# Optimization experiments

Hardware: AMD Instinct MI355X
Metric: run time of the kernel (lower is better)

## Reference

```python
import jax, jax.numpy as jnp
import numpy as np

N_NODES = 50000
N_HYPEREDGES = 50000
E = 320000
D = 256


def _prelu(x, a):
    return jnp.where(x >= 0, x, a * x)


def _hypergraph_conv(x, hei, W, b, num_nodes, num_edges):
    # PyG HypergraphConv, use_attention=False, heads=1:
    # out = D^{-1} H B^{-1} H^T (X W^T) + b
    src = hei[0]  # node indices, [E]
    he = hei[1]   # hyperedge indices, [E]
    xw = x @ W.T  # [N, D] node transform (lin has no bias)
    ones = jnp.ones((hei.shape[1],), x.dtype)
    deg_n = jax.ops.segment_sum(ones, src, num_segments=num_nodes)   # node degree D
    deg_e = jax.ops.segment_sum(ones, he, num_segments=num_edges)    # hyperedge size B
    d_inv = jnp.where(deg_n > 0, 1.0 / deg_n, 0.0)
    b_inv = jnp.where(deg_e > 0, 1.0 / deg_e, 0.0)
    # node -> hyperedge aggregation, scaled by B^{-1}
    edge_feat = b_inv[:, None] * jax.ops.segment_sum(xw[src], he, num_segments=num_edges)  # [n_he, D]
    # hyperedge -> node aggregation, scaled by D^{-1}
    out = d_inv[:, None] * jax.ops.segment_sum(edge_feat[he], src, num_segments=num_nodes)  # [N, D]
    return out + b


def setup_inputs() -> dict:
    key = jax.random.key(0)
    ks = jax.random.split(key, 6)
    std = np.sqrt(2.0 / D)  # kaiming_normal
    x = jax.random.normal(ks[0], (N_NODES, D), dtype=jnp.float32)
    hyper_edge_index = jax.random.randint(ks[1], (2, E), 0, N_HYPEREDGES, dtype=jnp.int64)
    W1 = jax.random.normal(ks[2], (D, D), dtype=jnp.float32) * std
    b1 = jnp.zeros((D,), jnp.float32)
    W2 = jax.random.normal(ks[3], (D, D), dtype=jnp.float32) * std
    b2 = jnp.zeros((D,), jnp.float32)
    prelu_a = jnp.asarray(0.25, jnp.float32)
    return {"x": x, "W1": W1, "b1": b1, "W2": W2, "b2": b2,
            "prelu_a": prelu_a, "hyper_edge_index": hyper_edge_index}


def reference(x, W1, b1, W2, b2, prelu_a, hyper_edge_index):
    out = _hypergraph_conv(x, hyper_edge_index, W1, b1, N_NODES, N_HYPEREDGES)
    out = _prelu(out, prelu_a)
    out = _hypergraph_conv(out, hyper_edge_index, W2, b2, N_NODES, N_HYPEREDGES)
    out = out + x  # residual
    out = _prelu(out, prelu_a)
    return out
```

## Files before the change

kernel.cpp:

```cpp
#include <hip/hip_runtime.h>

#define NN    50000
#define NHE   50000
#define NEDGE 320000
#define DD    256

#define SB    1024
#define NBLK  ((NN + SB - 1) / SB)
#define CNTB  ((NEDGE / 4 + 255) / 256)
#define XCB   (NN * DD / 2048)

typedef float f32x4 __attribute__((ext_vector_type(4)));
typedef short short8 __attribute__((ext_vector_type(8)));

static __device__ __forceinline__ unsigned short f2b(float f) {
    union { float f; unsigned u; } c; c.f = f;
    unsigned u = c.u;
    u += 0x7fffu + ((u >> 16) & 1u);
    return (unsigned short)(u >> 16);
}
static __device__ __forceinline__ float b2f_lo(unsigned v) {
    union { unsigned u; float f; } c; c.u = v << 16; return c.f;
}
static __device__ __forceinline__ float b2f_hi(unsigned v) {
    union { unsigned u; float f; } c; c.u = v & 0xffff0000u; return c.f;
}
static __device__ __forceinline__ unsigned pack2(float a, float b) {
    return (unsigned)f2b(a) | ((unsigned)f2b(b) << 16);
}

static __device__ __forceinline__ void glds16(const unsigned short* g, unsigned short* l) {
    __builtin_amdgcn_global_load_lds((const __attribute__((address_space(1))) unsigned int*)g,
                                     (__attribute__((address_space(3))) unsigned int*)l,
                                     16, 0, 0);
}

__global__ __launch_bounds__(256) void k_count_cvt(const int* __restrict__ src,
                                                   const int* __restrict__ he,
                                                   int* __restrict__ cnt_n,
                                                   int* __restrict__ cnt_e,
                                                   int* __restrict__ rank_n,
                                                   int* __restrict__ rank_e,
                                                   const float* __restrict__ w1,
                                                   const float* __restrict__ w2,
                                                   unsigned short* __restrict__ o1,
                                                   unsigned short* __restrict__ o2,
                                                   const float* __restrict__ x,
                                                   unsigned short* __restrict__ xb) {
    int bx = blockIdx.x;
    if (bx >= CNTB + 128) {
        int t = (bx - CNTB - 128) * 256 + threadIdx.x;
        const float4* p = (const float4*)x + (size_t)t * 2;
        float4 a = p[0], b = p[1];
        uint4 o;
        o.x = pack2(a.x, a.y); o.y = pack2(a.z, a.w);
        o.z = pack2(b.x, b.y); o.w = pack2(b.z, b.w);
        ((uint4*)xb)[t] = o;
        return;
    }
    if (bx >= CNTB) {
        int t = (bx - CNTB) * 256 + threadIdx.x;
        const int n4 = DD * DD / 4;
        const float* s = (t < n4) ? w1 : w2;
        unsigned short* d = (t < n4) ? o1 : o2;
        int i = (t < n4) ? t : t - n4;
        float4 v = ((const float4*)s)[i];
        uint2 o;
        o.x = pack2(v.x, v.y);
        o.y = pack2(v.z, v.w);
        ((uint2*)d)[i] = o;
        return;
    }
    int t  = bx * 256 + threadIdx.x;
    int e0 = t * 4;
    if (e0 >= NEDGE) return;
    int4 s = *(const int4*)(src + e0);
    int4 h = *(const int4*)(he + e0);
    int4 rn, re;
    rn.x = atomicAdd(&cnt_n[s.x], 1);
    rn.y = atomicAdd(&cnt_n[s.y], 1);
    rn.z = atomicAdd(&cnt_n[s.z], 1);
    rn.w = atomicAdd(&cnt_n[s.w], 1);
    re.x = atomicAdd(&cnt_e[h.x], 1);
    re.y = atomicAdd(&cnt_e[h.y], 1);
    re.z = atomicAdd(&cnt_e[h.z], 1);
    re.w = atomicAdd(&cnt_e[h.w], 1);
    *(int4*)(rank_n + e0) = rn;
    *(int4*)(rank_e + e0) = re;
}

__global__ __launch_bounds__(256) void k_scan(const int* __restrict__ cnt_n,
                                              const int* __restrict__ cnt_e,
                                              int* __restrict__ off_n,
                                              int* __restrict__ off_e) {
    int b   = blockIdx.x;
    int seg = b / NBLK, lb = b % NBLK;
    const int* cnt = seg ? cnt_e : cnt_n;
    int* off = seg ? off_e : off_n;
    int t = threadIdx.x;

    int pre = lb * SB;
    int s = 0;
    for (int i = t * 4; i < pre; i += 1024) {
        int4 c = *(const int4*)(cnt + i);
        s += c.x + c.y + c.z + c.w;
    }
    __shared__ int red[256];
    red[t] = s;
    __syncthreads();
    for (int o = 128; o > 0; o >>= 1) {
        if (t < o) red[t] += red[t + o];
        __syncthreads();
    }
    int base = red[0];

    int idx = pre + t * 4;
    int v[4];
    int tsum = 0;
#pragma unroll
    for (int j = 0; j < 4; ++j) {
        v[j] = (idx + j < NN) ? cnt[idx + j] : 0;
        tsum += v[j];
    }
    __shared__ int sc[256];
    sc[t] = tsum;
    __syncthreads();
    for (int o = 1; o < 256; o <<= 1) {
        int val = (t >= o) ? sc[t - o] : 0;
        __syncthreads();
        sc[t] += val;
        __syncthreads();
    }
    int p = base + sc[t] - tsum;
#pragma unroll
    for (int j = 0; j < 4; ++j) {
        if (idx + j < NN) off[idx + j] = p;
        p += v[j];
    }
    if (lb == NBLK - 1 && t == 255) off[NN] = base + sc[255];
}

__global__ __launch_bounds__(256) void k_fill(const int* __restrict__ src,
                                              const int* __restrict__ he,
                                              const int* __restrict__ off_n,
                                              const int* __restrict__ off_e,
                                              const int* __restrict__ rank_n,
                                              const int* __restrict__ rank_e,
                                              int* __restrict__ adj_n,
                                              int* __restrict__ adj_e) {
    int t  = blockIdx.x * 256 + threadIdx.x;
    int e0 = t * 4;
    if (e0 >= NEDGE) return;
    int4 s  = *(const int4*)(src + e0);
    int4 h  = *(const int4*)(he + e0);
    int4 rn = *(const int4*)(rank_n + e0);
    int4 re = *(const int4*)(rank_e + e0);
    int on0 = off_n[s.x], on1 = off_n[s.y], on2 = off_n[s.z], on3 = off_n[s.w];
    int oe0 = off_e[h.x], oe1 = off_e[h.y], oe2 = off_e[h.z], oe3 = off_e[h.w];
    adj_n[on0 + rn.x] = h.x;
    adj_n[on1 + rn.y] = h.y;
    adj_n[on2 + rn.z] = h.z;
    adj_n[on3 + rn.w] = h.w;
    adj_e[oe0 + re.x] = s.x;
    adj_e[oe1 + re.y] = s.y;
    adj_e[oe2 + re.z] = s.z;
    adj_e[oe3 + re.w] = s.w;
}

__global__ __launch_bounds__(1024) void k_gemm(const unsigned short* __restrict__ Av,
                                               const unsigned short* __restrict__ Wb,
                                               unsigned short* __restrict__ Cb) {
    __shared__ __align__(16) unsigned short Bs[128 * 256];
    const int t    = threadIdx.x;
    const int lane = t & 63;
    const int wave = t >> 6;
    const int n0   = (blockIdx.x & 1) * 128;
    const int fr   = lane & 15;
    const int fq   = lane >> 4;

#pragma unroll
    for (int q = 0; q < 4; ++q) {
        int row   = q * 32 + wave * 2 + (lane >> 5);
        int chunk = lane & 31;
        glds16(Wb + (size_t)(n0 + row) * DD + ((chunk ^ (row & 7)) * 8),
               Bs + q * 8192 + wave * 512);
    }

    int mchunk = (blockIdx.x >> 1) * 16 + wave;
    int m0  = mchunk * 16;
    int m0c = (m0 + 16 <= NN) ? m0 : NN - 16;
    short8 af[8];
    {
        const unsigned short* p = Av + (size_t)(m0c + fr) * DD + fq * 8;
#pragma unroll
        for (int kc = 0; kc < 8; ++kc)
            af[kc] = *(const short8*)(p + kc * 32);
    }

    __syncthreads();
    if (m0 >= NN) return;

    f32x4 acc[8] = {};
#pragma unroll
    for (int kc = 0; kc < 8; ++kc) {
#pragma unroll
        for (int nt = 0; nt < 8; ++nt) {
            int r  = nt * 16 + fr;
            int ch = (kc * 4 + fq) ^ (fr & 7);
            short8 bf = *(const short8*)(Bs + r * 256 + ch * 8);
            acc[nt] = __builtin_amdgcn_mfma_f32_16x16x32_bf16(af[kc], bf, acc[nt], 0, 0, 0);
        }
    }

#pragma unroll
    for (int nt = 0; nt < 8; ++nt)
#pragma unroll
        for (int i = 0; i < 4; ++i)
            Cb[(size_t)(m0 + fq * 4 + i) * DD + n0 + nt * 16 + fr] = f2b(acc[nt][i]);
}

static __device__ __forceinline__ void acc8(float* a, uint4 v) {
    a[0] += b2f_lo(v.x); a[1] += b2f_hi(v.x);
    a[2] += b2f_lo(v.y); a[3] += b2f_hi(v.y);
    a[4] += b2f_lo(v.z); a[5] += b2f_hi(v.z);
    a[6] += b2f_lo(v.w); a[7] += b2f_hi(v.w);
}
static __device__ __forceinline__ void gather8(const unsigned short* __restrict__ srcb,
                                               const int* __restrict__ adj,
                                               int b, int e, int sl, float* a) {
#pragma unroll
    for (int i = 0; i < 8; ++i) a[i] = 0.f;
    for (int i = b; i < e; i += 8) {
        int g0 = adj[i];
        int g[8];
        g[0] = g0;
#pragma unroll
        for (int j = 1; j < 8; ++j) g[j] = (i + j < e) ? adj[i + j] : g0;
        uint4 v[8];
#pragma unroll
        for (int j = 0; j < 8; ++j)
            v[j] = *(const uint4*)(srcb + (size_t)g[j] * DD + sl * 8);
        acc8(a, v[0]);
#pragma unroll
        for (int j = 1; j < 8; ++j)
            if (i + j < e) acc8(a, v[j]);
    }
}

__global__ __launch_bounds__(256) void k_gather_edge_b(const unsigned short* __restrict__ xw,
                                                       unsigned short* __restrict__ ef,
                                                       const int* __restrict__ off,
                                                       const int* __restrict__ adj) {
    int tid = blockIdx.x * 256 + threadIdx.x;
    int w = tid >> 5;
    int sl = tid & 31;
    if (w >= NHE) return;
    int b = off[w], e = off[w + 1];
    float a[8];
    gather8(xw, adj, b, e, sl, a);
    float sc = (e > b) ? 1.f / (float)(e - b) : 0.f;
    uint4 o;
    o.x = pack2(a[0] * sc, a[1] * sc);
    o.y = pack2(a[2] * sc, a[3] * sc);
    o.z = pack2(a[4] * sc, a[5] * sc);
    o.w = pack2(a[6] * sc, a[7] * sc);
    *(uint4*)(ef + (size_t)w * DD + sl * 8) = o;
}

__global__ __launch_bounds__(256) void k_gather_node_mid_b(const unsigned short* __restrict__ ef,
                                                           unsigned short* __restrict__ h,
                                                           const int* __restrict__ off,
                                                           const int* __restrict__ adj,
                                                           const float* __restrict__ bias,
                                                           const float* __restrict__ aP) {
    int tid = blockIdx.x * 256 + threadIdx.x;
    int w = tid >> 5;
    int sl = tid & 31;
    if (w >= NN) return;
    int b = off[w], e = off[w + 1];
    float a[8];
    gather8(ef, adj, b, e, sl, a);
    float sc = (e > b) ? 1.f / (float)(e - b) : 0.f;
    float al = *aP;
    float4 bb0 = ((const float4*)bias)[sl * 2];
    float4 bb1 = ((const float4*)bias)[sl * 2 + 1];
    float r[8];
    r[0] = a[0] * sc + bb0.x; r[1] = a[1] * sc + bb0.y;
    r[2] = a[2] * sc + bb0.z; r[3] = a[3] * sc + bb0.w;
    r[4] = a[4] * sc + bb1.x; r[5] = a[5] * sc + bb1.y;
    r[6] = a[6] * sc + bb1.z; r[7] = a[7] * sc + bb1.w;
#pragma unroll
    for (int i = 0; i < 8; ++i) r[i] = (r[i] >= 0.f) ? r[i] : al * r[i];
    uint4 o;
    o.x = pack2(r[0], r[1]);
    o.y = pack2(r[2], r[3]);
    o.z = pack2(r[4], r[5]);
    o.w = pack2(r[6], r[7]);
    *(uint4*)(h + (size_t)w * DD + sl * 8) = o;
}

__global__ __launch_bounds__(256) void k_gather_node_final_b(const unsigned short* __restrict__ ef,
                                                             const float* __restrict__ x,
                                                             float* __restrict__ out,
                                                             const int* __restrict__ off,
                                                             const int* __restrict__ adj,
                                                             const float* __restrict__ bias,
                                                             const float* __restrict__ aP) {
    int tid = blockIdx.x * 256 + threadIdx.x;
    int w = tid >> 5;
    int sl = tid & 31;
    if (w >= NN) return;
    int b = off[w], e = off[w + 1];
    float a[8];
    gather8(ef, adj, b, e, sl, a);
    float sc = (e > b) ? 1.f / (float)(e - b) : 0.f;
    float al = *aP;
    float4 bb0 = ((const float4*)bias)[sl * 2];
    float4 bb1 = ((const float4*)bias)[sl * 2 + 1];
    const float* xp = x + (size_t)w * DD + sl * 8;
    float4 xv0 = *(const float4*)xp;
    float4 xv1 = *(const float4*)(xp + 4);
    float r[8];
    r[0] = a[0] * sc + bb0.x + xv0.x; r[1] = a[1] * sc + bb0.y + xv0.y;
    r[2] = a[2] * sc + bb0.z + xv0.z; r[3] = a[3] * sc + bb0.w + xv0.w;
    r[4] = a[4] * sc + bb1.x + xv1.x; r[5] = a[5] * sc + bb1.y + xv1.y;
    r[6] = a[6] * sc + bb1.z + xv1.z; r[7] = a[7] * sc + bb1.w + xv1.w;
#pragma unroll
    for (int i = 0; i < 8; ++i) r[i] = (r[i] >= 0.f) ? r[i] : al * r[i];
    float* op = out + (size_t)w * DD + sl * 8;
    *(float4*)op = make_float4(r[0], r[1], r[2], r[3]);
    *(float4*)(op + 4) = make_float4(r[4], r[5], r[6], r[7]);
}

extern "C" void kernel_launch(void* const* d_in, const int* in_sizes, int n_in,
                              void* d_out, int out_size, void* d_ws, size_t ws_size,
                              hipStream_t stream) {
    const float* x       = (const float*)d_in[0];
    const float* W1      = (const float*)d_in[1];
    const float* b1      = (const float*)d_in[2];
    const float* W2      = (const float*)d_in[3];
    const float* b2      = (const float*)d_in[4];
    const float* prelu_a = (const float*)d_in[5];
    const int*   hei     = (const int*)d_in[6];
    const int* idx_src = hei;
    const int* idx_he  = hei + NEDGE;

    float* out = (float*)d_out;
    unsigned short* B1 = (unsigned short*)d_ws;
    unsigned short* B2 = B1 + (size_t)NN * DD;
    int* off_n  = (int*)(B2 + (size_t)NN * DD);
    int* off_e  = off_n + NN + 1;
    int* cnt_n  = off_e + NHE + 1;
    int* cnt_e  = cnt_n + NN;
    int* adj_n  = cnt_e + NHE;
    int* adj_e  = adj_n + NEDGE;
    int* rank_n = adj_e + NEDGE;
    int* rank_e = rank_n + NEDGE;
    unsigned short* w1b = (unsigned short*)d_out;
    unsigned short* w2b = w1b + DD * DD;

    const int gblocks = (NN * 32 + 255) / 256;
    const int gemmb   = 2 * (NN / 16 / 16 + 1);

    hipMemsetAsync(cnt_n, 0, sizeof(int) * (NN + NHE), stream);
    k_count_cvt<<<CNTB + 128 + XCB, 256, 0, stream>>>(idx_src, idx_he, cnt_n, cnt_e,
                                                      rank_n, rank_e, W1, W2, w1b, w2b,
                                                      x, B2);
    k_scan<<<2 * NBLK, 256, 0, stream>>>(cnt_n, cnt_e, off_n, off_e);
    k_fill<<<CNTB, 256, 0, stream>>>(idx_src, idx_he, off_n, off_e,
                                     rank_n, rank_e, adj_n, adj_e);

    k_gemm<<<gemmb, 1024, 0, stream>>>(B2, w1b, B1);
    k_gather_edge_b<<<gblocks, 256, 0, stream>>>(B1, B2, off_e, adj_e);
    k_gather_node_mid_b<<<gblocks, 256, 0, stream>>>(B2, B1, off_n, adj_n, b1, prelu_a);

    k_gemm<<<gemmb, 1024, 0, stream>>>(B1, w2b, B2);
    k_gather_edge_b<<<gblocks, 256, 0, stream>>>(B2, B1, off_e, adj_e);
    k_gather_node_final_b<<<gblocks, 256, 0, stream>>>(B1, x, out, off_n, adj_n, b2, prelu_a);
}
```

Measured before the change: 306.4 us.

## Split degree counters into four sub-buckets to reduce atomic contention

The per-node and per-hyperedge degree counters are replaced by four interleaved sub-counters per index, chosen from the block id, so concurrent atomics from different blocks land on different addresses. The scan now also emits a base offset for each sub-bucket, and the fill kernel uses those bases plus the recorded rank to place adjacency entries. The counters live in the B1 workspace before the GEMM overwrites it. This trades atomic contention for a fourfold larger counter array, a larger memset, and more scan traffic.

Result: slower. 323.8 us (+5.7%).

```diff
diff --git a/kernel.cpp b/kernel.cpp
--- a/kernel.cpp
+++ b/kernel.cpp
@@ -9,6 +9,7 @@
 #define NBLK  ((NN + SB - 1) / SB)
 #define CNTB  ((NEDGE / 4 + 255) / 256)
 #define XCB   (NN * DD / 2048)
+#define NBKT  100000
 
 typedef float f32x4 __attribute__((ext_vector_type(4)));
 typedef short short8 __attribute__((ext_vector_type(8)));
@@ -37,8 +38,7 @@
 
 __global__ __launch_bounds__(256) void k_count_cvt(const int* __restrict__ src,
                                                    const int* __restrict__ he,
-                                                   int* __restrict__ cnt_n,
-                                                   int* __restrict__ cnt_e,
+                                                   int* __restrict__ cntI,
                                                    int* __restrict__ rank_n,
                                                    int* __restrict__ rank_e,
                                                    const float* __restrict__ w1,
@@ -74,35 +74,37 @@
     int t  = bx * 256 + threadIdx.x;
     int e0 = t * 4;
     if (e0 >= NEDGE) return;
+    int r = bx & 3;
     int4 s = *(const int4*)(src + e0);
     int4 h = *(const int4*)(he + e0);
     int4 rn, re;
-    rn.x = atomicAdd(&cnt_n[s.x], 1);
-    rn.y = atomicAdd(&cnt_n[s.y], 1);
-    rn.z = atomicAdd(&cnt_n[s.z], 1);
-    rn.w = atomicAdd(&cnt_n[s.w], 1);
-    re.x = atomicAdd(&cnt_e[h.x], 1);
-    re.y = atomicAdd(&cnt_e[h.y], 1);
-    re.z = atomicAdd(&cnt_e[h.z], 1);
-    re.w = atomicAdd(&cnt_e[h.w], 1);
+    rn.x = atomicAdd(&cntI[s.x * 4 + r], 1);
+    rn.y = atomicAdd(&cntI[s.y * 4 + r], 1);
+    rn.z = atomicAdd(&cntI[s.z * 4 + r], 1);
+    rn.w = atomicAdd(&cntI[s.w * 4 + r], 1);
+    re.x = atomicAdd(&cntI[(50000 + h.x) * 4 + r], 1);
+    re.y = atomicAdd(&cntI[(50000 + h.y) * 4 + r], 1);
+    re.z = atomicAdd(&cntI[(50000 + h.z) * 4 + r], 1);
+    re.w = atomicAdd(&cntI[(50000 + h.w) * 4 + r], 1);
     *(int4*)(rank_n + e0) = rn;
     *(int4*)(rank_e + e0) = re;
 }
 
-__global__ __launch_bounds__(256) void k_scan(const int* __restrict__ cnt_n,
-                                              const int* __restrict__ cnt_e,
+__global__ __launch_bounds__(256) void k_scan(const int* __restrict__ cntI,
                                               int* __restrict__ off_n,
-                                              int* __restrict__ off_e) {
+                                              int* __restrict__ off_e,
+                                              int* __restrict__ baseI) {
     int b   = blockIdx.x;
     int seg = b / NBLK, lb = b % NBLK;
-    const int* cnt = seg ? cnt_e : cnt_n;
+    const int4* cnt4 = (const int4*)cntI + (size_t)seg * 50000;
+    int4* base4 = (int4*)baseI + (size_t)seg * 50000;
     int* off = seg ? off_e : off_n;
     int t = threadIdx.x;
 
     int pre = lb * SB;
     int s = 0;
-    for (int i = t * 4; i < pre; i += 1024) {
-        int4 c = *(const int4*)(cnt + i);
+    for (int i = t; i < pre; i += 256) {
+        int4 c = cnt4[i];
         s += c.x + c.y + c.z + c.w;
     }
     __shared__ int red[256];
@@ -115,12 +117,14 @@
     int base = red[0];
 
     int idx = pre + t * 4;
-    int v[4];
+    int4 cv[4];
+    int tot[4];
     int tsum = 0;
 #pragma unroll
     for (int j = 0; j < 4; ++j) {
-        v[j] = (idx + j < NN) ? cnt[idx + j] : 0;
-        tsum += v[j];
+        cv[j] = (idx + j < NN) ? cnt4[idx + j] : make_int4(0, 0, 0, 0);
+        tot[j] = cv[j].x + cv[j].y + cv[j].z + cv[j].w;
+        tsum += tot[j];
     }
     __shared__ int sc[256];
     sc[t] = tsum;
@@ -134,16 +138,23 @@
     int p = base + sc[t] - tsum;
 #pragma unroll
     for (int j = 0; j < 4; ++j) {
-        if (idx + j < NN) off[idx + j] = p;
-        p += v[j];
+        if (idx + j < NN) {
+            off[idx + j] = p;
+            int4 b4;
+            b4.x = p;
+            b4.y = b4.x + cv[j].x;
+            b4.z = b4.y + cv[j].y;
+            b4.w = b4.z + cv[j].z;
+            base4[idx + j] = b4;
+        }
+        p += tot[j];
     }
     if (lb == NBLK - 1 && t == 255) off[NN] = base + sc[255];
 }
 
 __global__ __launch_bounds__(256) void k_fill(const int* __restrict__ src,
                                               const int* __restrict__ he,
-                                              const int* __restrict__ off_n,
-                                              const int* __restrict__ off_e,
+                                              const int* __restrict__ baseI,
                                               const int* __restrict__ rank_n,
                                               const int* __restrict__ rank_e,
                                               int* __restrict__ adj_n,
@@ -151,20 +162,27 @@
     int t  = blockIdx.x * 256 + threadIdx.x;
     int e0 = t * 4;
     if (e0 >= NEDGE) return;
+    int r = (e0 >> 10) & 3;
     int4 s  = *(const int4*)(src + e0);
     int4 h  = *(const int4*)(he + e0);
     int4 rn = *(const int4*)(rank_n + e0);
     int4 re = *(const int4*)(rank_e + e0);
-    int on0 = off_n[s.x], on1 = off_n[s.y], on2 = off_n[s.z], on3 = off_n[s.w];
-    int oe0 = off_e[h.x], oe1 = off_e[h.y], oe2 = off_e[h.z], oe3 = off_e[h.w];
-    adj_n[on0 + rn.x] = h.x;
-    adj_n[on1 + rn.y] = h.y;
-    adj_n[on2 + rn.z] = h.z;
-    adj_n[on3 + rn.w] = h.w;
-    adj_e[oe0 + re.x] = s.x;
-    adj_e[oe1 + re.y] = s.y;
-    adj_e[oe2 + re.z] = s.z;
-    adj_e[oe3 + re.w] = s.w;
+    int pn0 = baseI[s.x * 4 + r] + rn.x;
+    int pn1 = baseI[s.y * 4 + r] + rn.y;
+    int pn2 = baseI[s.z * 4 + r] + rn.z;
+    int pn3 = baseI[s.w * 4 + r] + rn.w;
+    int pe0 = baseI[(50000 + h.x) * 4 + r] + re.x;
+    int pe1 = baseI[(50000 + h.y) * 4 + r] + re.y;
+    int pe2 = baseI[(50000 + h.z) * 4 + r] + re.z;
+    int pe3 = baseI[(50000 + h.w) * 4 + r] + re.w;
+    adj_n[pn0] = h.x;
+    adj_n[pn1] = h.y;
+    adj_n[pn2] = h.z;
+    adj_n[pn3] = h.w;
+    adj_e[pe0] = s.x;
+    adj_e[pe1] = s.y;
+    adj_e[pe2] = s.z;
+    adj_e[pe3] = s.w;
 }
 
 __global__ __launch_bounds__(1024) void k_gemm(const unsigned short* __restrict__ Av,
@@ -348,26 +366,26 @@
     float* out = (float*)d_out;
     unsigned short* B1 = (unsigned short*)d_ws;
     unsigned short* B2 = B1 + (size_t)NN * DD;
-    int* off_n  = (int*)(B2 + (size_t)NN * DD);
-    int* off_e  = off_n + NN + 1;
-    int* cnt_n  = off_e + NHE + 1;
-    int* cnt_e  = cnt_n + NN;
-    int* adj_n  = cnt_e + NHE;
+    int* cntI   = (int*)B1;
+    int* baseI  = cntI + 4 * NBKT;
+    int* adj_n  = (int*)(B2 + (size_t)NN * DD);
     int* adj_e  = adj_n + NEDGE;
     int* rank_n = adj_e + NEDGE;
     int* rank_e = rank_n + NEDGE;
+    int* off_n  = rank_e + NEDGE;
+    int* off_e  = off_n + NN + 1;
     unsigned short* w1b = (unsigned short*)d_out;
     unsigned short* w2b = w1b + DD * DD;
 
     const int gblocks = (NN * 32 + 255) / 256;
     const int gemmb   = 2 * (NN / 16 / 16 + 1);
 
-    hipMemsetAsync(cnt_n, 0, sizeof(int) * (NN + NHE), stream);
-    k_count_cvt<<<CNTB + 128 + XCB, 256, 0, stream>>>(idx_src, idx_he, cnt_n, cnt_e,
+    hipMemsetAsync(cntI, 0, sizeof(int) * 4 * NBKT, stream);
+    k_count_cvt<<<CNTB + 128 + XCB, 256, 0, stream>>>(idx_src, idx_he, cntI,
                                                       rank_n, rank_e, W1, W2, w1b, w2b,
                                                       x, B2);
-    k_scan<<<2 * NBLK, 256, 0, stream>>>(cnt_n, cnt_e, off_n, off_e);
-    k_fill<<<CNTB, 256, 0, stream>>>(idx_src, idx_he, off_n, off_e,
+    k_scan<<<2 * NBLK, 256, 0, stream>>>(cntI, off_n, off_e, baseI);
+    k_fill<<<CNTB, 256, 0, stream>>>(idx_src, idx_he, baseI,
                                      rank_n, rank_e, adj_n, adj_e);
 
     k_gemm<<<gemmb, 1024, 0, stream>>>(B2, w1b, B1);
```
